# Performance work log

Measured on AMD Instinct MI355X. Metric: run time of the kernel, lower is better.

Reference implementation:

```python
import jax, jax.numpy as jnp
import numpy as np

TEMPERATURE = 5.0

def setup_inputs() -> dict:
    key = jax.random.key(0)
    k1, k2 = jax.random.split(key)
    B, D = 8192, 128
    features = jax.random.normal(k1, (B, D), dtype=jnp.float32)
    labels = jax.random.randint(k2, (B,), 0, 100, dtype=jnp.int64)
    return {"features": features, "labels": labels, "fac_label": 3}


def reference(features, labels, fac_label):
    # features: [B, D], labels: [B]
    B = features.shape[0]
    # positive-pair mask; note original's mask_scale row-copy loop is a no-op,
    # so mask_scale == mask, and mask_cross_feature == ones (fac_label unused in effect)
    mask = (labels[:, None] == labels[None, :]).astype(features.dtype)  # [B, B]

    sim = jnp.matmul(features, features.T) / TEMPERATURE  # [B, B]
    logits_max = jax.lax.stop_gradient(jnp.max(sim, axis=1, keepdims=True))
    logits = sim - logits_max

    # remove self-contrast (diagonal)
    logits_mask = 1.0 - jnp.eye(B, dtype=features.dtype)
    mask = mask * logits_mask

    exp_logits = jnp.exp(logits) * logits_mask
    log_prob = logits - jnp.log(1e-12 + exp_logits.sum(axis=1, keepdims=True))

    mean_log_prob_pos_mask = (mask * log_prob).sum(axis=1)  # [B]
    # vectorized form of the per-element reciprocal loop: 1/count where count>0 else 0
    cnt = mask.sum(axis=1)
    recip = jnp.where(cnt == 0, 0.0, 1.0 / jnp.where(cnt == 0, 1.0, cnt))

    loss = -(mean_log_prob_pos_mask * recip).mean()
    return loss
```

## Files before the change

kernel.cpp:

```cpp
#include <hip/hip_runtime.h>


#define BN 8192
#define DK 128
#define INV_T 0.2f
#define C1F 0.28853901f
#define C40F 27.7258872f

#define TILES 1056
#define PSLOTS 64

#define NCLS 100
#define PB 128
#define PROWS (BN / PB)

#define OFF_FB    0
#define OFF_PART  (2 * 1024 * 1024)
#define OFF_G     (OFF_PART + PSLOTS * BN * 4)
#define OFF_HIST  (OFF_G + NCLS * DK * 4)
#define OFF_BSUM  (OFF_HIST + 512)
#define OFF_CTR   (OFF_BSUM + 256)

typedef __attribute__((ext_vector_type(8))) short bf16x8;
typedef __attribute__((ext_vector_type(4))) float f32x4;

__device__ __forceinline__ unsigned short f2bf(float f) {
    unsigned u = __builtin_bit_cast(unsigned, f);
    u += 0x7fffu + ((u >> 16) & 1u);
    return (unsigned short)(u >> 16);
}

__device__ __forceinline__ float fexp2(float x) {
#if __has_builtin(__builtin_amdgcn_exp2f)
    return __builtin_amdgcn_exp2f(x);
#else
    float r; asm("v_exp_f32 %0, %1" : "=v"(r) : "v"(x)); return r;
#endif
}

__device__ __forceinline__ void load_lds16(const void* g, void* l) {
    __builtin_amdgcn_global_load_lds(
        (const __attribute__((address_space(1))) unsigned int*)g,
        (__attribute__((address_space(3))) unsigned int*)l, 16, 0, 0);
}

__global__ __launch_bounds__(256) void zero_kernel(float* __restrict__ G,
                                                   int* __restrict__ hist,
                                                   unsigned int* __restrict__ ctr) {
    const int t = threadIdx.x;
    float4* g4 = (float4*)G;
#pragma unroll
    for (int k = 0; k < (NCLS * DK / 4 + 255) / 256; ++k) {
        const int idx = k * 256 + t;
        if (idx < NCLS * DK / 4) g4[idx] = make_float4(0.f, 0.f, 0.f, 0.f);
    }
    if (t < NCLS) hist[t] = 0;
    if (t == 0) *ctr = 0u;
}

__global__ __launch_bounds__(256) void prep_kernel(const float* __restrict__ F,
                                                   const int* __restrict__ labels,
                                                   unsigned short* __restrict__ Fb,
                                                   float* __restrict__ part,
                                                   float* __restrict__ G,
                                                   int* __restrict__ hist) {
    const int t  = threadIdx.x;
    const int b  = blockIdx.x;
    const int r0 = b * PROWS;

    {
        float4* pz = (float4*)part + (size_t)b * (PSLOTS * BN / 4 / PB);
#pragma unroll
        for (int k = 0; k < PSLOTS * BN / 4 / PB / 256; ++k)
            pz[k * 256 + t] = make_float4(0.f, 0.f, 0.f, 0.f);
    }

    const float4* F4  = (const float4*)F + (size_t)b * (PROWS * DK / 4);
    ushort4*      Fb4 = (ushort4*)Fb + (size_t)b * (PROWS * DK / 4);
#pragma unroll
    for (int k = 0; k < PROWS * DK / 4 / 256; ++k) {
        float4 v = F4[k * 256 + t];
        ushort4 o;
        o.x = f2bf(v.x); o.y = f2bf(v.y); o.z = f2bf(v.z); o.w = f2bf(v.w);
        Fb4[k * 256 + t] = o;
    }

    __shared__ int   ll[PROWS];
    __shared__ int   lh[NCLS];
    __shared__ float gl[2][NCLS][DK];
    float4* gl4 = (float4*)gl;
    if (t < NCLS) lh[t] = 0;
    if (t < PROWS) ll[t] = labels[r0 + t];
#pragma unroll
    for (int k = 0; k < 2 * NCLS * DK / 4 / 256; ++k)
        gl4[k * 256 + t] = make_float4(0.f, 0.f, 0.f, 0.f);
    __syncthreads();

    if (t < PROWS) atomicAdd(&lh[ll[t]], 1);

    {
        const int half = t >> 7, col = t & 127;
        const int rb   = half * (PROWS / 2);
        for (int rr = 0; rr < PROWS / 2; ++rr) {
            const int lr = rb + rr;
            gl[half][ll[lr]][col] += F[(size_t)(r0 + lr) * DK + col];
        }
    }
    __syncthreads();

    if (t < NCLS && lh[t]) atomicAdd(&hist[t], lh[t]);
    const float* gl0 = (const float*)gl;
#pragma unroll
    for (int k = 0; k < NCLS * DK / 256; ++k) {
        const int idx = k * 256 + t;
        const int c   = idx >> 7;
        if (lh[c]) atomicAdd(&G[idx], gl0[idx] + gl0[NCLS * DK + idx]);
    }
}

template <bool DIAGT>
__device__ __forceinline__ void supcon_tile(const short* __restrict__ Fb,
                                            float* __restrict__ part,
                                            int bx, int cy, char* smem) {
    const int t    = threadIdx.x;
    const int wave = t >> 6, lane = t & 63;
    const int quad = lane >> 4, l16 = lane & 15;
    const int rowBase = bx * 128 + wave * 32;
    const int colBase = cy * 256;

    const char* Btile = (const char*)Fb + (size_t)colBase * 256;
    const int   gso   = (t & 15) * 256 + (t >> 6) * 64 + ((t >> 4) & 3) * 16;
    char*       ldsw  = smem + wave * 1024;

#pragma unroll
    for (int tt = 0; tt < 4; ++tt)
        load_lds16(Btile + tt * 4096 + gso, ldsw + tt * 4096);

    bf16x8 a[2][4];
#pragma unroll
    for (int rt = 0; rt < 2; ++rt)
#pragma unroll
        for (int kt = 0; kt < 4; ++kt)
            a[rt][kt] = *(const bf16x8*)(Fb + (size_t)(rowBase + rt * 16 + l16) * DK
                                            + kt * 32 + quad * 8);

    float Zs[2][4];
#pragma unroll
    for (int rt = 0; rt < 2; ++rt)
#pragma unroll
        for (int r = 0; r < 4; ++r) Zs[rt][r] = 0.f;
    float Zcol[4];

    const int    roffb   = quad * 256 + l16 * 16;
    float* const colpart = part + (size_t)(32 + (bx >> 1)) * BN + colBase;

    __syncthreads();

#pragma unroll
    for (int g = 0; g < 4; ++g) {
        if (g < 3) {
            char* dsth = smem + ((g + 1) & 1) * 16384 + wave * 1024;
#pragma unroll
            for (int tt = 0; tt < 4; ++tt)
                load_lds16(Btile + (size_t)((g + 1) * 4 + tt) * 4096 + gso,
                           dsth + tt * 4096);
        }
        const char* srch = smem + (g & 1) * 16384;
#pragma unroll
        for (int tt = 0; tt < 4; ++tt) {
            const int jt = g * 4 + tt;
            bf16x8 bb[4];
#pragma unroll
            for (int kt = 0; kt < 4; ++kt)
                bb[kt] = *(const bf16x8*)(srch + tt * 4096 + kt * 1024 + roffb);
            float Zc0 = 0.f, Zc1 = 0.f;
#pragma unroll
            for (int rt = 0; rt < 2; ++rt) {
                f32x4 acc = {0.f, 0.f, 0.f, 0.f};
#pragma unroll
                for (int kt = 0; kt < 4; ++kt)
                    acc = __builtin_amdgcn_mfma_f32_16x16x32_bf16(a[rt][kt], bb[kt],
                                                                  acc, 0, 0, 0);
#pragma unroll
                for (int r = 0; r < 4; ++r) {
                    float e = fexp2(fmaf(acc[r], C1F, -40.0f));
                    if (DIAGT) {
                        if (colBase + jt * 16 + l16 == rowBase + rt * 16 + quad * 4 + r)
                            e = 0.f;
                    }
                    Zs[rt][r] += e;
                    if (!DIAGT) { if (rt == 0) Zc0 += e; else Zc1 += e; }
                }
            }
            if (!DIAGT) {
                float Zc = Zc0 + Zc1;
                Zc += __shfl_xor(Zc, 16);
                Zc += __shfl_xor(Zc, 32);
                Zcol[tt] = Zc;
            }
        }
        if (g < 3) __syncthreads();
        if (!DIAGT && quad == 0) {
#pragma unroll
            for (int tt = 0; tt < 4; ++tt)
                atomicAdd(colpart + (g * 4 + tt) * 16 + l16, Zcol[tt]);
        }
    }

#pragma unroll
    for (int rt = 0; rt < 2; ++rt)
#pragma unroll
        for (int r = 0; r < 4; ++r) {
            float zz = Zs[rt][r];
#pragma unroll
            for (int h = 1; h < 16; h <<= 1) zz += __shfl_xor(zz, h);
            if (l16 == 0)
                part[(size_t)cy * BN + rowBase + rt * 16 + quad * 4 + r] = zz;
        }
}

__global__ __launch_bounds__(256) void supcon_main(const short* __restrict__ Fb,
                                                   float* __restrict__ part) {
    __shared__ alignas(16) char smem[32768];
    const int bid = blockIdx.x;
    int k0 = (int)sqrtf((float)bid);
    while ((k0 + 1) * (k0 + 1) <= bid) ++k0;
    while (k0 * k0 > bid) --k0;
    int bx, cy;
    if (bid < k0 * k0 + k0) { bx = 2 * k0 - 1; cy = bid - k0 * k0; }
    else                    { bx = 2 * k0;     cy = bid - k0 * k0 - k0; }
    if (cy == (bx >> 1)) supcon_tile<true >(Fb, part, bx, cy, smem);
    else                 supcon_tile<false>(Fb, part, bx, cy, smem);
}

__global__ __launch_bounds__(256) void supcon_finalize(const float* __restrict__ F,
                                                       const int* __restrict__ labels,
                                                       const float* __restrict__ part,
                                                       const float* __restrict__ G,
                                                       const int* __restrict__ hist,
                                                       float* __restrict__ bsums,
                                                       unsigned int* __restrict__ ctr,
                                                       float* __restrict__ out) {
    const int t  = threadIdx.x;
    const int i  = blockIdx.x * 256 + t;
    const int c2 = blockIdx.x;

    float Zm = 0.f;
#pragma unroll 8
    for (int k = 0; k < 32; ++k) {
        const int slot = (k <= c2) ? k : 32 + k;
        Zm += part[(size_t)slot * BN + i];
    }

    const int   lbl = labels[i];
    const float cnt = (float)(hist[lbl] - 1);

    const float4* fr = (const float4*)(F + (size_t)i * DK);
    const float4* gr = (const float4*)(G + lbl * DK);
    float dot = 0.f, nrm = 0.f;
#pragma unroll 8
    for (int k = 0; k < DK / 4; ++k) {
        const float4 av = fr[k], gv = gr[k];
        dot += av.x * gv.x + av.y * gv.y + av.z * gv.z + av.w * gv.w;
        nrm += av.x * av.x + av.y * av.y + av.z * av.z + av.w * av.w;
    }

    const float mt = nrm * INV_T;
    const float A  = (dot - nrm) * INV_T;
    float term = 0.f;
    if (cnt > 0.5f)
        term = (A - cnt * mt) / cnt - __logf(1e-12f + Zm * __expf(C40F - mt));

    float sum = term;
#pragma unroll
    for (int h = 1; h < 64; h <<= 1) sum += __shfl_xor(sum, h);
    __shared__ float ss[4];
    if ((t & 63) == 0) ss[t >> 6] = sum;
    __syncthreads();
    if (t == 0) {
        bsums[blockIdx.x] = ss[0] + ss[1] + ss[2] + ss[3];
        __threadfence();
        const unsigned old = atomicAdd(ctr, 1u);
        if (old == (BN / 256) - 1) {
            __threadfence();
            float tot = 0.f;
            const volatile float* vb = bsums;
            for (int c = 0; c < BN / 256; ++c) tot += vb[c];
            out[0] = -tot * (1.0f / BN);
        }
    }
}

extern "C" void kernel_launch(void* const* d_in, const int* in_sizes, int n_in,
                              void* d_out, int out_size, void* d_ws, size_t ws_size,
                              hipStream_t stream) {
    const float* F      = (const float*)d_in[0];
    const int*   labels = (const int*)d_in[1];
    float* out = (float*)d_out;
    char*  ws  = (char*)d_ws;

    unsigned short* Fb    = (unsigned short*)(ws + OFF_FB);
    float*          part  = (float*)(ws + OFF_PART);
    float*          G     = (float*)(ws + OFF_G);
    int*            hist  = (int*)(ws + OFF_HIST);
    float*          bsums = (float*)(ws + OFF_BSUM);
    unsigned int*   ctr   = (unsigned int*)(ws + OFF_CTR);

    zero_kernel<<<1, 256, 0, stream>>>(G, hist, ctr);
    prep_kernel<<<PB, 256, 0, stream>>>(F, labels, Fb, part, G, hist);
    supcon_main<<<TILES, 256, 0, stream>>>((const short*)Fb, part);
    supcon_finalize<<<BN / 256, 256, 0, stream>>>(F, labels, part, G, hist,
                                                  bsums, ctr, out);
}
```

Measured before the change: 121.2 us.

## Fold class-sum computation into main kernel as extra rider blocks and drop zero kernel

Removes the separate zero kernel and moves the per-class feature sums and histogram out of prep_kernel into 100 extra blocks appended to the main GEMM-tile grid. Each of these blocks scans all labels and writes its class sum directly, so no atomics or zeroing are needed. prep_kernel now zeroes only the upper half of the partial slots, and finalize runs with 128 blocks of 64 threads plus a shuffle-based final reduction. The goal is to save one launch and shorten prep. The cost is that the rider blocks each do a serial gather over their class rows, and this may lengthen the tail of the main kernel.

```diff
diff --git a/kernel.cpp b/kernel.cpp
--- a/kernel.cpp
+++ b/kernel.cpp
@@ -14,12 +14,14 @@
 #define PB 128
 #define PROWS (BN / PB)
 
+#define FBLKS 128
+
 #define OFF_FB    0
 #define OFF_PART  (2 * 1024 * 1024)
 #define OFF_G     (OFF_PART + PSLOTS * BN * 4)
 #define OFF_HIST  (OFF_G + NCLS * DK * 4)
 #define OFF_BSUM  (OFF_HIST + 512)
-#define OFF_CTR   (OFF_BSUM + 256)
+#define OFF_CTR   (OFF_BSUM + 1024)
 
 typedef __attribute__((ext_vector_type(8))) short bf16x8;
 typedef __attribute__((ext_vector_type(4))) float f32x4;
@@ -44,35 +46,19 @@
         (__attribute__((address_space(3))) unsigned int*)l, 16, 0, 0);
 }
 
-__global__ __launch_bounds__(256) void zero_kernel(float* __restrict__ G,
-                                                   int* __restrict__ hist,
+__global__ __launch_bounds__(256) void prep_kernel(const float* __restrict__ F,
+                                                   unsigned short* __restrict__ Fb,
+                                                   float* __restrict__ part,
                                                    unsigned int* __restrict__ ctr) {
     const int t = threadIdx.x;
-    float4* g4 = (float4*)G;
-#pragma unroll
-    for (int k = 0; k < (NCLS * DK / 4 + 255) / 256; ++k) {
-        const int idx = k * 256 + t;
-        if (idx < NCLS * DK / 4) g4[idx] = make_float4(0.f, 0.f, 0.f, 0.f);
-    }
-    if (t < NCLS) hist[t] = 0;
-    if (t == 0) *ctr = 0u;
-}
-
-__global__ __launch_bounds__(256) void prep_kernel(const float* __restrict__ F,
-                                                   const int* __restrict__ labels,
-                                                   unsigned short* __restrict__ Fb,
-                                                   float* __restrict__ part,
-                                                   float* __restrict__ G,
-                                                   int* __restrict__ hist) {
-    const int t  = threadIdx.x;
-    const int b  = blockIdx.x;
-    const int r0 = b * PROWS;
+    const int b = blockIdx.x;
+
+    if (b == 0 && t == 0) *ctr = 0u;
 
     {
-        float4* pz = (float4*)part + (size_t)b * (PSLOTS * BN / 4 / PB);
-#pragma unroll
-        for (int k = 0; k < PSLOTS * BN / 4 / PB / 256; ++k)
-            pz[k * 256 + t] = make_float4(0.f, 0.f, 0.f, 0.f);
+        float4* pz = (float4*)(part + (size_t)32 * BN) + (size_t)b * 512;
+        pz[t]       = make_float4(0.f, 0.f, 0.f, 0.f);
+        pz[t + 256] = make_float4(0.f, 0.f, 0.f, 0.f);
     }
 
     const float4* F4  = (const float4*)F + (size_t)b * (PROWS * DK / 4);
@@ -83,38 +69,6 @@
         ushort4 o;
         o.x = f2bf(v.x); o.y = f2bf(v.y); o.z = f2bf(v.z); o.w = f2bf(v.w);
         Fb4[k * 256 + t] = o;
-    }
-
-    __shared__ int   ll[PROWS];
-    __shared__ int   lh[NCLS];
-    __shared__ float gl[2][NCLS][DK];
-    float4* gl4 = (float4*)gl;
-    if (t < NCLS) lh[t] = 0;
-    if (t < PROWS) ll[t] = labels[r0 + t];
-#pragma unroll
-    for (int k = 0; k < 2 * NCLS * DK / 4 / 256; ++k)
-        gl4[k * 256 + t] = make_float4(0.f, 0.f, 0.f, 0.f);
-    __syncthreads();
-
-    if (t < PROWS) atomicAdd(&lh[ll[t]], 1);
-
-    {
-        const int half = t >> 7, col = t & 127;
-        const int rb   = half * (PROWS / 2);
-        for (int rr = 0; rr < PROWS / 2; ++rr) {
-            const int lr = rb + rr;
-            gl[half][ll[lr]][col] += F[(size_t)(r0 + lr) * DK + col];
-        }
-    }
-    __syncthreads();
-
-    if (t < NCLS && lh[t]) atomicAdd(&hist[t], lh[t]);
-    const float* gl0 = (const float*)gl;
-#pragma unroll
-    for (int k = 0; k < NCLS * DK / 256; ++k) {
-        const int idx = k * 256 + t;
-        const int c   = idx >> 7;
-        if (lh[c]) atomicAdd(&G[idx], gl0[idx] + gl0[NCLS * DK + idx]);
     }
 }
 
@@ -219,10 +173,51 @@
         }
 }
 
+__device__ __forceinline__ void class_rider(const float* __restrict__ F,
+                                            const int* __restrict__ labels,
+                                            float* __restrict__ G,
+                                            int* __restrict__ hist,
+                                            int c, char* smem) {
+    const int t    = threadIdx.x;
+    int*      rows = (int*)smem;
+    int*      nrs  = (int*)(smem + 8192);
+    float*    gh   = (float*)(smem + 8192 + 64);
+
+    if (t == 0) *nrs = 0;
+    __syncthreads();
+#pragma unroll
+    for (int k = 0; k < BN / 256; ++k) {
+        const int r = k * 256 + t;
+        if (labels[r] == c) {
+            const int idx = atomicAdd(nrs, 1);
+            if (idx < 2048) rows[idx] = r;
+        }
+    }
+    __syncthreads();
+    const int n = *nrs;
+
+    const int half = t >> 7, col = t & 127;
+    float acc = 0.f;
+    for (int j = half; j < n; j += 2)
+        acc += F[(size_t)rows[j] * DK + col];
+    gh[t] = acc;
+    __syncthreads();
+    if (t < DK) G[c * DK + t] = gh[t] + gh[t + DK];
+    if (t == 0) hist[c] = n;
+}
+
 __global__ __launch_bounds__(256) void supcon_main(const short* __restrict__ Fb,
-                                                   float* __restrict__ part) {
+                                                   float* __restrict__ part,
+                                                   const float* __restrict__ F,
+                                                   const int* __restrict__ labels,
+                                                   float* __restrict__ G,
+                                                   int* __restrict__ hist) {
     __shared__ alignas(16) char smem[32768];
     const int bid = blockIdx.x;
+    if (bid >= TILES) {
+        class_rider(F, labels, G, hist, bid - TILES, smem);
+        return;
+    }
     int k0 = (int)sqrtf((float)bid);
     while ((k0 + 1) * (k0 + 1) <= bid) ++k0;
     while (k0 * k0 > bid) --k0;
@@ -233,17 +228,17 @@
     else                 supcon_tile<false>(Fb, part, bx, cy, smem);
 }
 
-__global__ __launch_bounds__(256) void supcon_finalize(const float* __restrict__ F,
-                                                       const int* __restrict__ labels,
-                                                       const float* __restrict__ part,
-                                                       const float* __restrict__ G,
-                                                       const int* __restrict__ hist,
-                                                       float* __restrict__ bsums,
-                                                       unsigned int* __restrict__ ctr,
-                                                       float* __restrict__ out) {
+__global__ __launch_bounds__(64) void supcon_finalize(const float* __restrict__ F,
+                                                      const int* __restrict__ labels,
+                                                      const float* __restrict__ part,
+                                                      const float* __restrict__ G,
+                                                      const int* __restrict__ hist,
+                                                      float* __restrict__ bsums,
+                                                      unsigned int* __restrict__ ctr,
+                                                      float* __restrict__ out) {
     const int t  = threadIdx.x;
-    const int i  = blockIdx.x * 256 + t;
-    const int c2 = blockIdx.x;
+    const int i  = blockIdx.x * 64 + t;
+    const int c2 = blockIdx.x >> 2;
 
     float Zm = 0.f;
 #pragma unroll 8
@@ -274,20 +269,21 @@
     float sum = term;
 #pragma unroll
     for (int h = 1; h < 64; h <<= 1) sum += __shfl_xor(sum, h);
-    __shared__ float ss[4];
-    if ((t & 63) == 0) ss[t >> 6] = sum;
-    __syncthreads();
+
+    __shared__ int lastf;
     if (t == 0) {
-        bsums[blockIdx.x] = ss[0] + ss[1] + ss[2] + ss[3];
+        bsums[blockIdx.x] = sum;
         __threadfence();
         const unsigned old = atomicAdd(ctr, 1u);
-        if (old == (BN / 256) - 1) {
-            __threadfence();
-            float tot = 0.f;
-            const volatile float* vb = bsums;
-            for (int c = 0; c < BN / 256; ++c) tot += vb[c];
-            out[0] = -tot * (1.0f / BN);
-        }
+        lastf = (old == FBLKS - 1);
+    }
+    __syncthreads();
+    if (lastf) {
+        const volatile float* vb = bsums;
+        float v = vb[t] + vb[t + 64];
+#pragma unroll
+        for (int h = 1; h < 64; h <<= 1) v += __shfl_xor(v, h);
+        if (t == 0) out[0] = -v * (1.0f / BN);
     }
 }
 
@@ -306,9 +302,9 @@
     float*          bsums = (float*)(ws + OFF_BSUM);
     unsigned int*   ctr   = (unsigned int*)(ws + OFF_CTR);
 
-    zero_kernel<<<1, 256, 0, stream>>>(G, hist, ctr);
-    prep_kernel<<<PB, 256, 0, stream>>>(F, labels, Fb, part, G, hist);
-    supcon_main<<<TILES, 256, 0, stream>>>((const short*)Fb, part);
-    supcon_finalize<<<BN / 256, 256, 0, stream>>>(F, labels, part, G, hist,
-                                                  bsums, ctr, out);
-}
+    prep_kernel<<<PB, 256, 0, stream>>>(F, Fb, part, ctr);
+    supcon_main<<<TILES + NCLS, 256, 0, stream>>>((const short*)Fb, part,
+                                                  F, labels, G, hist);
+    supcon_finalize<<<FBLKS, 64, 0, stream>>>(F, labels, part, G, hist,
+                                              bsums, ctr, out);
+}
```

After: 121.6 us. Within noise of the previous version (+0.4%).
